# Kernel tuning notes

Hardware: AMD Instinct MI355X
Metric: run time of the kernel (lower is better)

The kernel has to match this reference:

```python
import jax, jax.numpy as jnp
import numpy as np

N_HEAD = 8
D_MODEL = 1024   # also the sequence length L (the code requires L == d_model)
D_K = 256
D_V = 256
D_TRANS = 256
B = 32
KS = 13
PAD = 6
LN_EPS = 1e-3
TEMPER = float(np.sqrt(D_MODEL))


def conv1d(x, w, b):
    # x: (B, Cin, L), w: (Cout, Cin, K) torch layout, 'same' padding 6
    y = jax.lax.conv_general_dilated(
        x, w, window_strides=(1,), padding=[(PAD, PAD)],
        dimension_numbers=('NCH', 'OIH', 'NCH'))
    return y + b[None, :, None]


def setup_inputs() -> dict:
    key = jax.random.key(0)
    ks = jax.random.split(key, 16)
    n = lambda i, shape, s=1.0: jax.random.normal(ks[i], shape, jnp.float32) * s
    return {
        'q': n(0, (B, D_K, D_MODEL)),
        'k': n(1, (B, D_K, D_MODEL)),
        'v': n(2, (B, D_V, D_MODEL)),
        'cq_w': n(3, (D_TRANS, D_K, KS), 0.02), 'cq_b': jnp.zeros((D_TRANS,), jnp.float32),
        'ck_w': n(4, (D_TRANS, D_K, KS), 0.02), 'ck_b': jnp.zeros((D_TRANS,), jnp.float32),
        'cv_w': n(5, (D_TRANS, D_V, KS), 0.02), 'cv_b': jnp.zeros((D_TRANS,), jnp.float32),
        'w_qs': n(6, (N_HEAD, D_MODEL, D_TRANS), 0.02),
        'w_ks': n(7, (N_HEAD, D_MODEL, D_TRANS), 0.02),
        'w_vs': n(8, (N_HEAD, D_MODEL, D_TRANS), 0.02),
        'proj_w': n(9, (D_MODEL, N_HEAD * D_TRANS), 0.02),
        'proj_b': jnp.zeros((D_MODEL,), jnp.float32),
        'fc_w': n(10, (D_V, D_TRANS, KS), 0.02), 'fc_b': jnp.zeros((D_V,), jnp.float32),
        'ln_a': jnp.ones((D_MODEL,), jnp.float32),
        'ln_b': jnp.zeros((D_MODEL,), jnp.float32),
    }


def reference(q, k, v, cq_w, cq_b, ck_w, ck_b, cv_w, cv_b,
              w_qs, w_ks, w_vs, proj_w, proj_b, fc_w, fc_b, ln_a, ln_b):
    # Conv1d QKV "projections": (B, d_k, L) -> (B, d_trans, L)
    q_b = conv1d(q, cq_w, cq_b)
    k_b = conv1d(k, ck_w, ck_b)
    v_b = conv1d(v, cv_w, cv_b)

    # Per-head projection along the L (==d_model) axis:
    # torch: (H, B*d_trans, L) bmm (H, L, d_trans) -> (H*B, d_trans, d_trans)
    q_s = jnp.einsum('btl,hld->hbtd', q_b, w_qs)  # (H, B, Dt, Dt)
    k_s = jnp.einsum('btl,hld->hbtd', k_b, w_ks)
    v_s = jnp.einsum('btl,hld->hbtd', v_b, w_vs)

    # Scaled dot-product attention over the d_trans axis (eval mode: dropout off)
    scores = jnp.einsum('hbqd,hbkd->hbqk', q_s, k_s) / TEMPER
    attn = jax.nn.softmax(scores, axis=-1)
    out = jnp.einsum('hbqk,hbkd->hbqd', attn, v_s)  # (H, B, Dt, Dt)

    # torch: split heads along batch dim, concat along last -> (B, Dt, H*Dt)
    outputs = out.transpose(1, 2, 0, 3).reshape(B, D_TRANS, N_HEAD * D_TRANS)
    outputs = outputs @ proj_w.T + proj_b            # (B, Dt, d_model)
    outputs = conv1d(outputs, fc_w, fc_b)            # (B, d_v, d_model)

    # Custom LayerNorm over last axis with unbiased std and eps added to sigma
    z = outputs + q
    mu = jnp.mean(z, axis=-1, keepdims=True)
    sigma = jnp.std(z, axis=-1, ddof=1, keepdims=True)
    output = (z - mu) / (sigma + LN_EPS) * ln_a + ln_b

    attns = attn.reshape(N_HEAD * B, D_TRANS, D_TRANS)
    return output, attns
```

## Files before the change

### kernel.cpp

```cpp
#include <hip/hip_runtime.h>

typedef unsigned short u16;
typedef __attribute__((ext_vector_type(8))) short short8;
typedef __attribute__((ext_vector_type(4))) float f32x4;

__device__ __forceinline__ float bf2f(u16 x) {
  unsigned u = ((unsigned)x) << 16;
  return __builtin_bit_cast(float, u);
}
__device__ __forceinline__ u16 f2bf(float x) {
  unsigned u = __builtin_bit_cast(unsigned, x);
  u += 0x7fffu + ((u >> 16) & 1u);
  return (u16)(u >> 16);
}

__device__ __forceinline__ void gl2lds16(const u16* g, u16* l) {
  __builtin_amdgcn_global_load_lds(
      (const __attribute__((address_space(1))) unsigned*)g,
      (__attribute__((address_space(3))) unsigned*)l, 16, 0, 0);
}

__global__ void detect_kernel(const void* ln_a, unsigned* flag) {
  if (threadIdx.x == 0 && blockIdx.x == 0)
    *flag = (*(const unsigned*)ln_a == 0x3F800000u) ? 1u : 0u;
}

template <typename OutT>
__global__ __launch_bounds__(256) void gemm_kernel(
    const u16* __restrict__ A, const u16* __restrict__ B, OutT* __restrict__ C,
    const u16* __restrict__ bias, int K, int lda, int ldb, int ldc,
    long a0, long a1, long a2, long b0, long b1, long b2,
    long c0, long c1, long c2, int biasMid, float alpha) {
  const int tid = threadIdx.x;
  const int z = blockIdx.z;
  const int zlo = z & 31, zmid = (z >> 5) & 7, zhi = z >> 8;
  const u16* Ab = A + (long)zlo * a0 + (long)zmid * a1 + (long)zhi * a2;
  const u16* Bb = B + (long)zlo * b0 + (long)zmid * b1 + (long)zhi * b2;
  OutT* Cb = C + (long)zlo * c0 + (long)zmid * c1 + (long)zhi * c2;
  const int m0 = blockIdx.y * 128;
  const int n0 = blockIdx.x * 128;

  __shared__ __align__(16) u16 As[128 * 64];
  __shared__ __align__(16) u16 Bs[128 * 64];

  const int wave = tid >> 6;
  const int lane = tid & 63;

  const int rl = lane >> 3;
  const int jj = lane & 7;
  const u16* gA[4];
  const u16* gB[4];
  u16* lA[4];
  u16* lB[4];
#pragma unroll
  for (int c = 0; c < 4; c++) {
    const int row = wave * 32 + c * 8 + rl;
    const int q = jj ^ (row & 7);
    gA[c] = Ab + (long)(m0 + row) * lda + q * 8;
    gB[c] = Bb + (long)(n0 + row) * ldb + q * 8;
    lA[c] = As + (wave * 32 + c * 8) * 64;
    lB[c] = Bs + (wave * 32 + c * 8) * 64;
  }

  const int wm = (wave >> 1) * 64;
  const int wn = (wave & 1) * 64;
  const int quad = lane >> 4;
  const int r = lane & 15;
  int offA[4][2], offB[4][2];
#pragma unroll
  for (int i = 0; i < 4; i++) {
#pragma unroll
    for (int ks = 0; ks < 2; ks++) {
      const int rowA = wm + i * 16 + r;
      offA[i][ks] = rowA * 64 + ((ks * 4 + quad) ^ (rowA & 7)) * 8;
      const int rowB = wn + i * 16 + r;
      offB[i][ks] = rowB * 64 + ((ks * 4 + quad) ^ (rowB & 7)) * 8;
    }
  }

  f32x4 acc[4][4] = {};

  for (int k0 = 0; k0 < K; k0 += 64) {
    __syncthreads();
#pragma unroll
    for (int c = 0; c < 4; c++) {
      gl2lds16(gA[c] + k0, lA[c]);
      gl2lds16(gB[c] + k0, lB[c]);
    }
    __syncthreads();
#pragma unroll
    for (int ks = 0; ks < 2; ks++) {
      short8 af[4], bfr[4];
#pragma unroll
      for (int i = 0; i < 4; i++) af[i] = *(const short8*)(&As[offA[i][ks]]);
#pragma unroll
      for (int j = 0; j < 4; j++) bfr[j] = *(const short8*)(&Bs[offB[j][ks]]);
#pragma unroll
      for (int i = 0; i < 4; i++)
#pragma unroll
        for (int j = 0; j < 4; j++)
          acc[i][j] = __builtin_amdgcn_mfma_f32_16x16x32_bf16(af[i], bfr[j],
                                                              acc[i][j], 0, 0, 0);
    }
  }

  const u16* biasb = bias ? bias + (long)zmid * biasMid : nullptr;
#pragma unroll
  for (int i = 0; i < 4; i++) {
#pragma unroll
    for (int rr = 0; rr < 4; rr++) {
      const int mg = m0 + wm + i * 16 + quad * 4 + rr;
      const float bv = biasb ? bf2f(biasb[mg]) : 0.0f;
#pragma unroll
      for (int j = 0; j < 4; j++) {
        const int ng = n0 + wn + j * 16 + r;
        float val = acc[i][j][rr] * alpha + bv;
        if constexpr (__is_same(OutT, float))
          Cb[(long)mg * ldc + ng] = val;
        else
          Cb[(long)mg * ldc + ng] = f2bf(val);
      }
    }
  }
}

__global__ __launch_bounds__(256) void transpose_kernel(
    const void* __restrict__ i0, const void* __restrict__ i1,
    const void* __restrict__ i2, u16* __restrict__ out, int R, int C,
    long ostride, int ooff, int zdiv, const unsigned* __restrict__ flagp) {
  const bool f32 = *flagp != 0;
  __shared__ u16 t[64 * 68];
  const int z = blockIdx.z;
  const void* in = (z < zdiv) ? i0 : (z < 2 * zdiv) ? i1 : i2;
  const int zq = (z < zdiv) ? z : (z < 2 * zdiv) ? z - zdiv : z - 2 * zdiv;
  const long ibase = (long)zq * R * C;
  const int r0 = blockIdx.y * 64;
  const int c0 = blockIdx.x * 64;
  u16* ob = out + (long)z * ostride + ooff;
  const int tid = threadIdx.x;
#pragma unroll
  for (int i = 0; i < 4; i++) {
    const int vv = tid + i * 256;
    const int rr = vv >> 4;
    const int cc = (vv & 15) << 2;
    uint2 packed;
    if (f32) {
      const float4 fv = *(const float4*)((const float*)in + ibase +
                                         (long)(r0 + rr) * C + (c0 + cc));
      packed.x = (unsigned)f2bf(fv.x) | ((unsigned)f2bf(fv.y) << 16);
      packed.y = (unsigned)f2bf(fv.z) | ((unsigned)f2bf(fv.w) << 16);
    } else {
      packed = *(const uint2*)((const u16*)in + ibase + (long)(r0 + rr) * C +
                               (c0 + cc));
    }
    *(uint2*)(&t[rr * 68 + cc]) = packed;
  }
  __syncthreads();
#pragma unroll
  for (int i = 0; i < 4; i++) {
    const int vv = tid + i * 256;
    const int cc = vv >> 4;
    const int rr = (vv & 15) << 2;
    unsigned lo = (unsigned)t[rr * 68 + cc] | ((unsigned)t[(rr + 1) * 68 + cc] << 16);
    unsigned hi =
        (unsigned)t[(rr + 2) * 68 + cc] | ((unsigned)t[(rr + 3) * 68 + cc] << 16);
    uint2 val = {lo, hi};
    *(uint2*)(ob + (long)(c0 + cc) * R + (r0 + rr)) = val;
  }
}

__global__ __launch_bounds__(256) void pack_w_kernel(
    const void* __restrict__ w0, const void* __restrict__ w1,
    const void* __restrict__ w2, const void* __restrict__ w3,
    u16* __restrict__ out, const unsigned* __restrict__ flagp) {
  const bool f32 = *flagp != 0;
  const int y = blockIdx.y;
  const void* in = (y == 0) ? w0 : (y == 1) ? w1 : (y == 2) ? w2 : w3;
  u16* o = out + (long)y * 851968;
  const int t = blockIdx.x * 256 + threadIdx.x;
  const int co = t / 3328;
  const int rem = t - co * 3328;
  const int dk = rem >> 8;
  const int ci = rem & 255;
  const int src = co * 3328 + ci * 13 + dk;
  o[t] = f32 ? f2bf(((const float*)in)[src]) : ((const u16*)in)[src];
}

__global__ __launch_bounds__(256) void cvt_kernel(const void* __restrict__ in,
                                                  u16* __restrict__ out, long n,
                                                  const unsigned* __restrict__ flagp) {
  const bool f32 = *flagp != 0;
  const long i = ((long)blockIdx.x * 256 + threadIdx.x) * 8;
  if (i >= n) return;
  if (f32) {
    const float* p = (const float*)in + i;
    const float4 a = *(const float4*)p;
    const float4 b = *(const float4*)(p + 4);
    uint4 o;
    o.x = (unsigned)f2bf(a.x) | ((unsigned)f2bf(a.y) << 16);
    o.y = (unsigned)f2bf(a.z) | ((unsigned)f2bf(a.w) << 16);
    o.z = (unsigned)f2bf(b.x) | ((unsigned)f2bf(b.y) << 16);
    o.w = (unsigned)f2bf(b.z) | ((unsigned)f2bf(b.w) << 16);
    *(uint4*)(out + i) = o;
  } else {
    *(uint4*)(out + i) = *(const uint4*)((const u16*)in + i);
  }
}

__global__ __launch_bounds__(256) void bias_cvt_kernel(
    const void* __restrict__ s0, const void* __restrict__ s1,
    const void* __restrict__ s2, const void* __restrict__ s3,
    const void* __restrict__ s4, u16* __restrict__ out,
    const unsigned* __restrict__ flagp) {
  const bool f32 = *flagp != 0;
  const long i = threadIdx.x * 8;
  const void* src;
  long off;
  if (i < 256) { src = s0; off = i; }
  else if (i < 512) { src = s1; off = i - 256; }
  else if (i < 768) { src = s2; off = i - 512; }
  else if (i < 1024) { src = s3; off = i - 768; }
  else { src = s4; off = i - 1024; }
  if (f32) {
    const float* p = (const float*)src + off;
    const float4 a = *(const float4*)p;
    const float4 b = *(const float4*)(p + 4);
    uint4 o;
    o.x = (unsigned)f2bf(a.x) | ((unsigned)f2bf(a.y) << 16);
    o.y = (unsigned)f2bf(a.z) | ((unsigned)f2bf(a.w) << 16);
    o.z = (unsigned)f2bf(b.x) | ((unsigned)f2bf(b.y) << 16);
    o.w = (unsigned)f2bf(b.z) | ((unsigned)f2bf(b.w) << 16);
    *(uint4*)(out + i) = o;
  } else {
    *(uint4*)(out + i) = *(const uint4*)((const u16*)src + off);
  }
}

__global__ __launch_bounds__(256) void zeropad_kernel(u16* __restrict__ base,
                                                      long bstride, int nb) {
  const int t = blockIdx.x * 256 + threadIdx.x;
  if (t >= nb * 384) return;
  const int b = t / 384;
  const int rem = t - b * 384;
  const int rp = rem >> 5;
  const int col = (rem & 31) * 8;
  const int row = rp < 6 ? rp : 1024 + rp;
  uint4 zz = {0u, 0u, 0u, 0u};
  *(uint4*)(base + (long)b * bstride + row * 256 + col) = zz;
}

__global__ __launch_bounds__(256) void softmax_kernel(
    u16* __restrict__ sc, void* __restrict__ dout,
    const unsigned* __restrict__ flagp) {
  const bool f32 = *flagp != 0;
  const long row = (long)blockIdx.x * 4 + (threadIdx.x >> 6);
  const int lane = threadIdx.x & 63;
  const uint2 raw = *(const uint2*)(sc + row * 256 + lane * 4);
  float s0 = bf2f((u16)(raw.x & 0xffff)), s1 = bf2f((u16)(raw.x >> 16));
  float s2 = bf2f((u16)(raw.y & 0xffff)), s3 = bf2f((u16)(raw.y >> 16));
  float m = fmaxf(fmaxf(s0, s1), fmaxf(s2, s3));
  for (int o = 32; o > 0; o >>= 1) m = fmaxf(m, __shfl_xor(m, o, 64));
  float e0 = expf(s0 - m), e1 = expf(s1 - m), e2 = expf(s2 - m), e3 = expf(s3 - m);
  float sum = e0 + e1 + e2 + e3;
  for (int o = 32; o > 0; o >>= 1) sum += __shfl_xor(sum, o, 64);
  const float inv = 1.0f / sum;
  const float p0 = e0 * inv, p1 = e1 * inv, p2 = e2 * inv, p3 = e3 * inv;
  uint2 ov;
  ov.x = (unsigned)f2bf(p0) | ((unsigned)f2bf(p1) << 16);
  ov.y = (unsigned)f2bf(p2) | ((unsigned)f2bf(p3) << 16);
  *(uint2*)(sc + row * 256 + lane * 4) = ov;
  if (f32) {
    float4 o4 = {p0, p1, p2, p3};
    *(float4*)((float*)dout + 8388608 + row * 256 + lane * 4) = o4;
  } else {
    *(uint2*)((u16*)dout + 8388608 + row * 256 + lane * 4) = ov;
  }
}

__global__ __launch_bounds__(256) void ln_kernel(
    const float* __restrict__ fc, const void* __restrict__ qraw,
    const void* __restrict__ la, const void* __restrict__ lb,
    void* __restrict__ dout, const unsigned* __restrict__ flagp) {
  const bool f32 = *flagp != 0;
  __shared__ float red[4];
  const long row = blockIdx.x;
  const int tid = threadIdx.x;
  const int col = tid * 4;
  const float4 zf = *(const float4*)(fc + row * 1024 + col);
  float q0, q1, q2, q3;
  if (f32) {
    const float4 t = *(const float4*)((const float*)qraw + row * 1024 + col);
    q0 = t.x; q1 = t.y; q2 = t.z; q3 = t.w;
  } else {
    const uint2 qr = *(const uint2*)((const u16*)qraw + row * 1024 + col);
    q0 = bf2f((u16)(qr.x & 0xffff)); q1 = bf2f((u16)(qr.x >> 16));
    q2 = bf2f((u16)(qr.y & 0xffff)); q3 = bf2f((u16)(qr.y >> 16));
  }
  const float z0 = zf.x + q0, z1 = zf.y + q1, z2 = zf.z + q2, z3 = zf.w + q3;
  float s = z0 + z1 + z2 + z3;
  for (int o = 32; o > 0; o >>= 1) s += __shfl_xor(s, o, 64);
  if ((tid & 63) == 0) red[tid >> 6] = s;
  __syncthreads();
  const float mu = (red[0] + red[1] + red[2] + red[3]) * (1.0f / 1024.0f);
  __syncthreads();
  const float d0 = z0 - mu, d1 = z1 - mu, d2 = z2 - mu, d3 = z3 - mu;
  float ss = d0 * d0 + d1 * d1 + d2 * d2 + d3 * d3;
  for (int o = 32; o > 0; o >>= 1) ss += __shfl_xor(ss, o, 64);
  if ((tid & 63) == 0) red[tid >> 6] = ss;
  __syncthreads();
  const float var = (red[0] + red[1] + red[2] + red[3]) * (1.0f / 1023.0f);
  const float inv = 1.0f / (sqrtf(var) + 1e-3f);
  float a0, a1, a2, a3, b0, b1, b2, b3;
  if (f32) {
    const float4 ta = *(const float4*)((const float*)la + col);
    const float4 tb = *(const float4*)((const float*)lb + col);
    a0 = ta.x; a1 = ta.y; a2 = ta.z; a3 = ta.w;
    b0 = tb.x; b1 = tb.y; b2 = tb.z; b3 = tb.w;
  } else {
    const uint2 ta = *(const uint2*)((const u16*)la + col);
    const uint2 tb = *(const uint2*)((const u16*)lb + col);
    a0 = bf2f((u16)(ta.x & 0xffff)); a1 = bf2f((u16)(ta.x >> 16));
    a2 = bf2f((u16)(ta.y & 0xffff)); a3 = bf2f((u16)(ta.y >> 16));
    b0 = bf2f((u16)(tb.x & 0xffff)); b1 = bf2f((u16)(tb.x >> 16));
    b2 = bf2f((u16)(tb.y & 0xffff)); b3 = bf2f((u16)(tb.y >> 16));
  }
  const float o0 = d0 * inv * a0 + b0, o1 = d1 * inv * a1 + b1;
  const float o2v = d2 * inv * a2 + b2, o3 = d3 * inv * a3 + b3;
  if (f32) {
    float4 o4 = {o0, o1, o2v, o3};
    *(float4*)((float*)dout + row * 1024 + col) = o4;
  } else {
    uint2 o2;
    o2.x = (unsigned)f2bf(o0) | ((unsigned)f2bf(o1) << 16);
    o2.y = (unsigned)f2bf(o2v) | ((unsigned)f2bf(o3) << 16);
    *(uint2*)((u16*)dout + row * 1024 + col) = o2;
  }
}

enum : long {
  OWPQ = 0,
  OWPK = 851968,
  OWPV = 1703936,
  OWPFC = 2555904,
  OWQT = 3407872,
  OWKT = 5505024,
  OWVT = 7602176,
  OPW16 = 9699328,
  OBQKV = 11796480,
  OBFC = 11797248,
  OBPROJ = 11797504,
  OFLAG = 11798528,
  OQB = 11798536,
  OKB = 20187144,
  OVB = 28575752,
  OQS = 36964360,
  OKS = 53741576,
  OVST = 70518792,
  OXPAD = OQS,
  OSC = OQB,
  OOUTC = OQS,
  OPROJP = OKS,
  OFC = OVST,
};

extern "C" void kernel_launch(void* const* d_in, const int* in_sizes, int n_in,
                              void* d_out, int out_size, void* d_ws,
                              size_t ws_size, hipStream_t stream) {
  const void* q = d_in[0];
  const void* k = d_in[1];
  const void* v = d_in[2];
  const void* cq_w = d_in[3];
  const void* cq_b = d_in[4];
  const void* ck_w = d_in[5];
  const void* ck_b = d_in[6];
  const void* cv_w = d_in[7];
  const void* cv_b = d_in[8];
  const void* w_qs = d_in[9];
  const void* w_ks = d_in[10];
  const void* w_vs = d_in[11];
  const void* proj_w = d_in[12];
  const void* proj_b = d_in[13];
  const void* fc_w = d_in[14];
  const void* fc_b = d_in[15];
  const void* ln_a = d_in[16];
  const void* ln_b = d_in[17];

  u16* ws = (u16*)d_ws;
  unsigned* flag = (unsigned*)(ws + OFLAG);

  detect_kernel<<<1, 64, 0, stream>>>(ln_a, flag);

  pack_w_kernel<<<dim3(3328, 4), 256, 0, stream>>>(cq_w, ck_w, cv_w, fc_w,
                                                   ws + OWPQ, flag);
  transpose_kernel<<<dim3(4, 16, 24), 256, 0, stream>>>(
      w_qs, w_ks, w_vs, ws + OWQT, 1024, 256, 262144, 0, 8, flag);
  cvt_kernel<<<1024, 256, 0, stream>>>(proj_w, ws + OPW16, 2097152, flag);
  bias_cvt_kernel<<<1, 256, 0, stream>>>(cq_b, ck_b, cv_b, fc_b, proj_b,
                                         ws + OBQKV, flag);

  zeropad_kernel<<<144, 256, 0, stream>>>(ws + OXPAD, 265216, 96);
  transpose_kernel<<<dim3(16, 4, 96), 256, 0, stream>>>(
      q, k, v, ws + OXPAD, 256, 1024, 265216, 1536, 32, flag);

  gemm_kernel<u16><<<dim3(8, 2, 96), 256, 0, stream>>>(
      ws + OWPQ, ws + OXPAD, ws + OQB, ws + OBQKV, 3328, 3328, 256, 1024,
      0, 851968, 0, 265216, 8486912, 0, 262144, 8388608, 0, 256, 1.0f);

  gemm_kernel<u16><<<dim3(2, 2, 512), 256, 0, stream>>>(
      ws + OQB, ws + OWQT, ws + OQS, nullptr, 1024, 1024, 1024, 256,
      262144, 0, 8388608, 0, 262144, 2097152, 65536, 2097152, 16777216, 0, 1.0f);
  gemm_kernel<u16><<<dim3(2, 2, 256), 256, 0, stream>>>(
      ws + OWVT, ws + OVB, ws + OVST, nullptr, 1024, 1024, 1024, 256,
      0, 262144, 0, 262144, 0, 0, 65536, 2097152, 0, 0, 1.0f);

  gemm_kernel<u16><<<dim3(2, 2, 256), 256, 0, stream>>>(
      ws + OQS, ws + OKS, ws + OSC, nullptr, 256, 256, 256, 256,
      65536, 2097152, 0, 65536, 2097152, 0, 65536, 2097152, 0, 0, 0.03125f);

  softmax_kernel<<<16384, 256, 0, stream>>>(ws + OSC, d_out, flag);

  gemm_kernel<u16><<<dim3(2, 2, 256), 256, 0, stream>>>(
      ws + OSC, ws + OVST, ws + OOUTC, nullptr, 256, 256, 256, 2048,
      65536, 2097152, 0, 65536, 2097152, 0, 524288, 256, 0, 0, 1.0f);

  zeropad_kernel<<<48, 256, 0, stream>>>(ws + OPROJP, 265216, 32);
  gemm_kernel<u16><<<dim3(2, 8, 32), 256, 0, stream>>>(
      ws + OPW16, ws + OOUTC, ws + OPROJP + 1536, ws + OBPROJ, 2048, 2048, 2048,
      256, 0, 0, 0, 524288, 0, 0, 265216, 0, 0, 0, 1.0f);

  gemm_kernel<float><<<dim3(8, 2, 32), 256, 0, stream>>>(
      ws + OWPFC, ws + OPROJP, (float*)(ws + OFC), ws + OBFC, 3328, 3328, 256,
      1024, 0, 0, 0, 265216, 0, 0, 262144, 0, 0, 0, 1.0f);

  ln_kernel<<<8192, 256, 0, stream>>>((const float*)(ws + OFC), q, ln_a, ln_b,
                                      d_out, flag);

  (void)in_sizes; (void)n_in; (void)out_size; (void)ws_size;
}
```

Baseline: 875.8 us.

## Rewrite GEMM as 4-stage LDS ring pipeline with 256x128 tiles and 8 waves

Replaces the single-buffer, two-barrier GEMM main loop with a 4-slot dynamic-LDS ring that prefetches three K=32 tiles ahead. Each step issues the global-to-LDS copies under explicit vmcnt waits and raises wave priority around the MFMA block. Blocks grow to 512 threads computing 256x128 output tiles, so the grid's y dimension halves, and the LDS swizzle is reworked for 32-wide K slices. The aim is to hide global load latency and cut barrier stalls, at the cost of 96KB of LDS per block, which may limit occupancy. It also relies on hand-placed waitcnts being correct.

Result: faster. 815.8 us (-6.8%).

```diff
diff --git a/kernel.cpp b/kernel.cpp
--- a/kernel.cpp
+++ b/kernel.cpp
@@ -25,84 +25,108 @@
     *flag = (*(const unsigned*)ln_a == 0x3F800000u) ? 1u : 0u;
 }
 
+#define GEMM_TILE(T, DO_STAGE, VMCNT, ENDBAR)                                 \
+  {                                                                           \
+    const u16* ring_ = smem + ((T) & 3) * 12288;                              \
+    short8 af_[4], bq_[4];                                                    \
+    _Pragma("unroll") for (int i_ = 0; i_ < 4; i_++)                          \
+        af_[i_] = *(const short8*)(ring_ + offA[i_]);                         \
+    _Pragma("unroll") for (int j_ = 0; j_ < 4; j_++)                          \
+        bq_[j_] = *(const short8*)(ring_ + offB[j_]);                         \
+    if (DO_STAGE) stage_tile((T) + 3);                                        \
+    __builtin_amdgcn_s_barrier();                                             \
+    asm volatile("s_waitcnt lgkmcnt(0)" ::: "memory");                        \
+    __builtin_amdgcn_sched_barrier(0);                                        \
+    __builtin_amdgcn_s_setprio(1);                                            \
+    _Pragma("unroll") for (int i_ = 0; i_ < 4; i_++)                          \
+        _Pragma("unroll") for (int j_ = 0; j_ < 4; j_++)                      \
+            acc[i_][j_] = __builtin_amdgcn_mfma_f32_16x16x32_bf16(            \
+                af_[i_], bq_[j_], acc[i_][j_], 0, 0, 0);                      \
+    __builtin_amdgcn_s_setprio(0);                                            \
+    if ((VMCNT) == 6) asm volatile("s_waitcnt vmcnt(6)" ::: "memory");        \
+    else if ((VMCNT) == 3) asm volatile("s_waitcnt vmcnt(3)" ::: "memory");   \
+    else if ((VMCNT) == 0) asm volatile("s_waitcnt vmcnt(0)" ::: "memory");   \
+    if (ENDBAR) __builtin_amdgcn_s_barrier();                                 \
+  }
+
 template <typename OutT>
-__global__ __launch_bounds__(256) void gemm_kernel(
+__global__ __launch_bounds__(512, 2) void gemm_kernel(
     const u16* __restrict__ A, const u16* __restrict__ B, OutT* __restrict__ C,
     const u16* __restrict__ bias, int K, int lda, int ldb, int ldc,
     long a0, long a1, long a2, long b0, long b1, long b2,
     long c0, long c1, long c2, int biasMid, float alpha) {
+  extern __shared__ u16 smem[];
+
   const int tid = threadIdx.x;
   const int z = blockIdx.z;
   const int zlo = z & 31, zmid = (z >> 5) & 7, zhi = z >> 8;
   const u16* Ab = A + (long)zlo * a0 + (long)zmid * a1 + (long)zhi * a2;
   const u16* Bb = B + (long)zlo * b0 + (long)zmid * b1 + (long)zhi * b2;
   OutT* Cb = C + (long)zlo * c0 + (long)zmid * c1 + (long)zhi * c2;
-  const int m0 = blockIdx.y * 128;
+  const int m0 = blockIdx.y * 256;
   const int n0 = blockIdx.x * 128;
-
-  __shared__ __align__(16) u16 As[128 * 64];
-  __shared__ __align__(16) u16 Bs[128 * 64];
 
   const int wave = tid >> 6;
   const int lane = tid & 63;
 
-  const int rl = lane >> 3;
-  const int jj = lane & 7;
-  const u16* gA[4];
-  const u16* gB[4];
-  u16* lA[4];
-  u16* lB[4];
-#pragma unroll
-  for (int c = 0; c < 4; c++) {
-    const int row = wave * 32 + c * 8 + rl;
-    const int q = jj ^ (row & 7);
-    gA[c] = Ab + (long)(m0 + row) * lda + q * 8;
-    gB[c] = Bb + (long)(n0 + row) * ldb + q * 8;
-    lA[c] = As + (wave * 32 + c * 8) * 64;
-    lB[c] = Bs + (wave * 32 + c * 8) * 64;
-  }
+  const int lgrp = lane >> 3;
+  const int slot = lane & 7;
+  const u16* gsrc[3];
+  int ldsoff[3];
+#pragma unroll
+  for (int c = 0; c < 3; c++) {
+    const int L0 = (c < 2 ? c * 64 : 0) + wave * 8;
+    const int L = L0 + lgrp;
+    const int ls = slot ^ (L & 7);
+    const int row = 2 * L + (ls >> 2);
+    const int blk = ls & 3;
+    if (c < 2) {
+      gsrc[c] = Ab + (long)(m0 + row) * lda + blk * 8;
+      ldsoff[c] = L0 * 64;
+    } else {
+      gsrc[c] = Bb + (long)(n0 + row) * ldb + blk * 8;
+      ldsoff[c] = 8192 + L0 * 64;
+    }
+  }
+
+  auto stage_tile = [&](int t) {
+    u16* dst = smem + (t & 3) * 12288;
+    const long koff = (long)t * 32;
+#pragma unroll
+    for (int c = 0; c < 3; c++) gl2lds16(gsrc[c] + koff, dst + ldsoff[c]);
+  };
 
   const int wm = (wave >> 1) * 64;
   const int wn = (wave & 1) * 64;
   const int quad = lane >> 4;
   const int r = lane & 15;
-  int offA[4][2], offB[4][2];
+  int offA[4], offB[4];
 #pragma unroll
   for (int i = 0; i < 4; i++) {
-#pragma unroll
-    for (int ks = 0; ks < 2; ks++) {
-      const int rowA = wm + i * 16 + r;
-      offA[i][ks] = rowA * 64 + ((ks * 4 + quad) ^ (rowA & 7)) * 8;
-      const int rowB = wn + i * 16 + r;
-      offB[i][ks] = rowB * 64 + ((ks * 4 + quad) ^ (rowB & 7)) * 8;
-    }
+    const int rowA = wm + i * 16 + r;
+    const int lnA = rowA >> 1;
+    offA[i] = lnA * 64 + ((((rowA & 1) * 4 + quad) ^ (lnA & 7)) * 8);
+    const int rowB = wn + i * 16 + r;
+    const int lnB = rowB >> 1;
+    offB[i] = 8192 + lnB * 64 + ((((rowB & 1) * 4 + quad) ^ (lnB & 7)) * 8);
   }
 
   f32x4 acc[4][4] = {};
-
-  for (int k0 = 0; k0 < K; k0 += 64) {
-    __syncthreads();
-#pragma unroll
-    for (int c = 0; c < 4; c++) {
-      gl2lds16(gA[c] + k0, lA[c]);
-      gl2lds16(gB[c] + k0, lB[c]);
-    }
-    __syncthreads();
-#pragma unroll
-    for (int ks = 0; ks < 2; ks++) {
-      short8 af[4], bfr[4];
-#pragma unroll
-      for (int i = 0; i < 4; i++) af[i] = *(const short8*)(&As[offA[i][ks]]);
-#pragma unroll
-      for (int j = 0; j < 4; j++) bfr[j] = *(const short8*)(&Bs[offB[j][ks]]);
-#pragma unroll
-      for (int i = 0; i < 4; i++)
-#pragma unroll
-        for (int j = 0; j < 4; j++)
-          acc[i][j] = __builtin_amdgcn_mfma_f32_16x16x32_bf16(af[i], bfr[j],
-                                                              acc[i][j], 0, 0, 0);
-    }
-  }
+  const int nt = K >> 5;
+
+  stage_tile(0);
+  stage_tile(1);
+  stage_tile(2);
+  asm volatile("s_waitcnt vmcnt(6)" ::: "memory");
+  __builtin_amdgcn_s_barrier();
+
+  int t = 0;
+  for (; t < nt - 3; ++t) GEMM_TILE(t, true, 6, true);
+  GEMM_TILE(t, false, 3, true);
+  ++t;
+  GEMM_TILE(t, false, 0, true);
+  ++t;
+  GEMM_TILE(t, false, -1, false);
 
   const u16* biasb = bias ? bias + (long)zmid * biasMid : nullptr;
 #pragma unroll
@@ -388,6 +412,15 @@
   u16* ws = (u16*)d_ws;
   unsigned* flag = (unsigned*)(ws + OFLAG);
 
+  static int attr_done = 0;
+  if (!attr_done) {
+    hipFuncSetAttribute(reinterpret_cast<const void*>(&gemm_kernel<u16>),
+                        hipFuncAttributeMaxDynamicSharedMemorySize, 98304);
+    hipFuncSetAttribute(reinterpret_cast<const void*>(&gemm_kernel<float>),
+                        hipFuncAttributeMaxDynamicSharedMemorySize, 98304);
+    attr_done = 1;
+  }
+
   detect_kernel<<<1, 64, 0, stream>>>(ln_a, flag);
 
   pack_w_kernel<<<dim3(3328, 4), 256, 0, stream>>>(cq_w, ck_w, cv_w, fc_w,
@@ -402,33 +435,33 @@
   transpose_kernel<<<dim3(16, 4, 96), 256, 0, stream>>>(
       q, k, v, ws + OXPAD, 256, 1024, 265216, 1536, 32, flag);
 
-  gemm_kernel<u16><<<dim3(8, 2, 96), 256, 0, stream>>>(
+  gemm_kernel<u16><<<dim3(8, 1, 96), 512, 98304, stream>>>(
       ws + OWPQ, ws + OXPAD, ws + OQB, ws + OBQKV, 3328, 3328, 256, 1024,
       0, 851968, 0, 265216, 8486912, 0, 262144, 8388608, 0, 256, 1.0f);
 
-  gemm_kernel<u16><<<dim3(2, 2, 512), 256, 0, stream>>>(
+  gemm_kernel<u16><<<dim3(2, 1, 512), 512, 98304, stream>>>(
       ws + OQB, ws + OWQT, ws + OQS, nullptr, 1024, 1024, 1024, 256,
       262144, 0, 8388608, 0, 262144, 2097152, 65536, 2097152, 16777216, 0, 1.0f);
-  gemm_kernel<u16><<<dim3(2, 2, 256), 256, 0, stream>>>(
+  gemm_kernel<u16><<<dim3(2, 1, 256), 512, 98304, stream>>>(
       ws + OWVT, ws + OVB, ws + OVST, nullptr, 1024, 1024, 1024, 256,
       0, 262144, 0, 262144, 0, 0, 65536, 2097152, 0, 0, 1.0f);
 
-  gemm_kernel<u16><<<dim3(2, 2, 256), 256, 0, stream>>>(
+  gemm_kernel<u16><<<dim3(2, 1, 256), 512, 98304, stream>>>(
       ws + OQS, ws + OKS, ws + OSC, nullptr, 256, 256, 256, 256,
       65536, 2097152, 0, 65536, 2097152, 0, 65536, 2097152, 0, 0, 0.03125f);
 
   softmax_kernel<<<16384, 256, 0, stream>>>(ws + OSC, d_out, flag);
 
-  gemm_kernel<u16><<<dim3(2, 2, 256), 256, 0, stream>>>(
+  gemm_kernel<u16><<<dim3(2, 1, 256), 512, 98304, stream>>>(
       ws + OSC, ws + OVST, ws + OOUTC, nullptr, 256, 256, 256, 2048,
       65536, 2097152, 0, 65536, 2097152, 0, 524288, 256, 0, 0, 1.0f);
 
   zeropad_kernel<<<48, 256, 0, stream>>>(ws + OPROJP, 265216, 32);
-  gemm_kernel<u16><<<dim3(2, 8, 32), 256, 0, stream>>>(
+  gemm_kernel<u16><<<dim3(2, 4, 32), 512, 98304, stream>>>(
       ws + OPW16, ws + OOUTC, ws + OPROJP + 1536, ws + OBPROJ, 2048, 2048, 2048,
       256, 0, 0, 0, 524288, 0, 0, 265216, 0, 0, 0, 1.0f);
 
-  gemm_kernel<float><<<dim3(8, 2, 32), 256, 0, stream>>>(
+  gemm_kernel<float><<<dim3(8, 1, 32), 512, 98304, stream>>>(
       ws + OWPFC, ws + OPROJP, (float*)(ws + OFC), ws + OBFC, 3328, 3328, 256,
       1024, 0, 0, 0, 265216, 0, 0, 262144, 0, 0, 0, 1.0f);
 
```
